# Optimization experiments

Hardware: AMD Instinct MI355X
Metric: run time of the kernel (lower is better)

Reference implementation:

```python
import jax, jax.numpy as jnp
import numpy as np

EMBED = 2048
D_COMPR = 512
D_ROPE = 128
N_HEADS = 8
HEAD_DIM = D_COMPR // N_HEADS  # 64
B, S = 4, 2048


def _lin(x, w, b):
    # torch Linear: y = x @ w.T + b, w: [out, in]
    return jnp.einsum('bsi,oi->bso', x, w) + b


def _rope_emb(seq_len):
    inv_freq = 1.0 / (10000.0 ** (jnp.arange(0, D_ROPE, 2, dtype=jnp.float32) / D_ROPE))
    t = jnp.arange(seq_len, dtype=jnp.float32)
    freqs = jnp.einsum('i,j->ij', t, inv_freq)           # [S, D_ROPE/2]
    return jnp.concatenate([freqs, freqs], axis=-1)      # [S, D_ROPE]


def _apply_rope(x, emb):
    # x: [B, S, D_ROPE], emb: [S, D_ROPE]
    cos, sin = jnp.cos(emb), jnp.sin(emb)
    x1, x2 = jnp.split(x, 2, axis=-1)
    rot = jnp.concatenate([-x2, x1], axis=-1)
    return x * cos + rot * sin


def setup_inputs() -> dict:
    key = jax.random.key(0)
    ks = jax.random.split(key, 20)
    sc = 0.02
    inp = {'x': jax.random.normal(ks[0], (B, S, EMBED), dtype=jnp.float32)}
    def w(k, o, i):
        return jax.random.normal(k, (o, i), dtype=jnp.float32) * sc
    inp['CQ_w'] = w(ks[1], D_COMPR, EMBED); inp['CQ_b'] = jnp.zeros((D_COMPR,), jnp.float32)
    inp['CQC_w'] = w(ks[2], D_COMPR - D_ROPE, D_COMPR); inp['CQC_b'] = jnp.zeros((D_COMPR - D_ROPE,), jnp.float32)
    inp['CQR_w'] = w(ks[3], D_ROPE, EMBED); inp['CQR_b'] = jnp.zeros((D_ROPE,), jnp.float32)
    inp['CKV_w'] = w(ks[4], D_COMPR, EMBED); inp['CKV_b'] = jnp.zeros((D_COMPR,), jnp.float32)
    inp['CKR_w'] = w(ks[5], D_ROPE, EMBED); inp['CKR_b'] = jnp.zeros((D_ROPE,), jnp.float32)
    inp['CKC_w'] = w(ks[6], D_COMPR - D_ROPE, D_COMPR); inp['CKC_b'] = jnp.zeros((D_COMPR - D_ROPE,), jnp.float32)
    inp['CV_w'] = w(ks[7], D_COMPR, D_COMPR); inp['CV_b'] = jnp.zeros((D_COMPR,), jnp.float32)
    inp['OUT_w'] = w(ks[8], EMBED, D_COMPR); inp['OUT_b'] = jnp.zeros((EMBED,), jnp.float32)
    return inp


def reference(x, CQ_w, CQ_b, CQC_w, CQC_b, CQR_w, CQR_b, CKV_w, CKV_b,
              CKR_w, CKR_b, CKC_w, CKC_b, CV_w, CV_b, OUT_w, OUT_b):
    b, s, _ = x.shape
    gelu = lambda t: jax.nn.gelu(t, approximate=False)

    cq = gelu(_lin(x, CQ_w, CQ_b))                # [B,S,D_COMPR]
    cqc = _lin(cq, CQC_w, CQC_b)                  # [B,S,D_COMPR-D_ROPE]
    cqr = _lin(x, CQR_w, CQR_b)                   # [B,S,D_ROPE]
    ckv = gelu(_lin(x, CKV_w, CKV_b))             # [B,S,D_COMPR]
    ckr = _lin(x, CKR_w, CKR_b)                   # [B,S,D_ROPE]
    ckc = _lin(ckv, CKC_w, CKC_b)                 # [B,S,D_COMPR-D_ROPE]

    emb = _rope_emb(s)
    cqr = _apply_rope(cqr, emb)
    ckr = _apply_rope(ckr, emb)

    Q = gelu(jnp.concatenate([cqc, cqr], axis=-1))  # [B,S,D_COMPR]
    K = gelu(jnp.concatenate([ckc, ckr], axis=-1))
    V = _lin(ckv, CV_w, CV_b)

    Q = Q.reshape(b, s, N_HEADS, HEAD_DIM).transpose(0, 2, 1, 3)  # [B,H,S,D]
    K = K.reshape(b, s, N_HEADS, HEAD_DIM).transpose(0, 2, 1, 3)
    V = V.reshape(b, s, N_HEADS, HEAD_DIM).transpose(0, 2, 1, 3)

    scale = 1.0 / np.sqrt(HEAD_DIM).astype(np.float32)
    scores = jnp.einsum('bhqd,bhkd->bhqk', Q, K) * scale
    causal = jnp.triu(jnp.ones((s, s), dtype=bool), k=1)
    scores = jnp.where(causal[None, None], -jnp.inf, scores)
    attn = jax.nn.softmax(scores, axis=-1)
    out = jnp.einsum('bhqk,bhkd->bhqd', attn, V)
    out = out.transpose(0, 2, 1, 3).reshape(b, s, D_COMPR)
    return _lin(out, OUT_w, OUT_b)
```

## Files before the change

kernel.cpp:

```cpp
#include <hip/hip_runtime.h>
#include <cstdint>
#include <cstddef>

typedef unsigned short u16;
typedef short bf16x8 __attribute__((ext_vector_type(8)));
typedef float f32x4 __attribute__((ext_vector_type(4)));
typedef unsigned short u16x8 __attribute__((ext_vector_type(8)));

#define DEVINL __device__ __forceinline__

DEVINL u16 f2bf(float f) {
  union { float f; unsigned u; } v; v.f = f;
  unsigned r = v.u + 0x7FFFu + ((v.u >> 16) & 1u);
  return (u16)(r >> 16);
}
DEVINL float bf2f(u16 h) {
  union { unsigned u; float f; } v; v.u = ((unsigned)h) << 16;
  return v.f;
}
DEVINL float gelu_exact(float x) {
  return 0.5f * x * (1.0f + erff(x * 0.70710678118654752f));
}
DEVINL void gload_lds16(const void* g, void* l) {
  __builtin_amdgcn_global_load_lds(
      (const __attribute__((address_space(1))) void*)g,
      (__attribute__((address_space(3))) void*)l, 16, 0, 0);
}
DEVINL bf16x8 ld_frag(const u16* p) {
  return *reinterpret_cast<const bf16x8*>(p);
}

__global__ __launch_bounds__(256) void conv_f32_bf16(
    const float* __restrict__ src, u16* __restrict__ dst, int n4) {
  int i = blockIdx.x * 256 + threadIdx.x;
  int stride = gridDim.x * 256;
  for (; i < n4; i += stride) {
    float4 v = reinterpret_cast<const float4*>(src)[i];
    ushort4 o;
    o.x = f2bf(v.x); o.y = f2bf(v.y); o.z = f2bf(v.z); o.w = f2bf(v.w);
    reinterpret_cast<ushort4*>(dst)[i] = o;
  }
}

struct EpiSeg {
  const float* bias;
  void* dst;
  int stride;
  int col_start;
  int do_gelu;
};
struct EpiTable { EpiSeg s[4]; int nseg; };

template <int F32OUT>
__global__ __launch_bounds__(256) void gemm_bt(
    const u16* __restrict__ A, const u16* __restrict__ W, int K, EpiTable et) {
  __shared__ u16 As[128 * 32];
  __shared__ u16 Bs[128 * 32];
  const int tid = threadIdx.x;
  const int lane = tid & 63;
  const int wv = tid >> 6;
  const int g = lane >> 4;
  const int c = lane & 15;
  const int wr = (wv >> 1) * 64;
  const int wc = (wv & 1) * 64;
  const long long rowBase = (long long)blockIdx.x * 128;
  const long long colBase = (long long)blockIdx.y * 128;

  f32x4 acc[4][4];
#pragma unroll
  for (int m = 0; m < 4; ++m)
#pragma unroll
    for (int n = 0; n < 4; ++n) acc[m][n] = {0.f, 0.f, 0.f, 0.f};

  const int r0 = tid >> 2, sp0 = tid & 3;
  const int scol = (sp0 ^ ((r0 >> 1) & 3)) * 8;
  const u16* Ag = A + (rowBase + r0) * K + scol;
  const u16* Wg = W + (colBase + r0) * K + scol;
  u16* Al0 = As + tid * 8;
  u16* Al1 = As + (256 + tid) * 8;
  u16* Bl0 = Bs + tid * 8;
  u16* Bl1 = Bs + (256 + tid) * 8;
  const long long skip = 64LL * K;

  int aoff[4], boff[4];
#pragma unroll
  for (int m = 0; m < 4; ++m) {
    int row = wr + m * 16 + c;
    aoff[m] = row * 32 + ((g ^ ((row >> 1) & 3)) * 8);
    int rowb = wc + m * 16 + c;
    boff[m] = rowb * 32 + ((g ^ ((rowb >> 1) & 3)) * 8);
  }

  const int nk = K >> 5;
  for (int kt = 0; kt < nk; ++kt) {
    const int k0 = kt * 32;
    gload_lds16(Ag + k0, Al0);
    gload_lds16(Ag + skip + k0, Al1);
    gload_lds16(Wg + k0, Bl0);
    gload_lds16(Wg + skip + k0, Bl1);
    __syncthreads();
    bf16x8 a[4], b[4];
#pragma unroll
    for (int m = 0; m < 4; ++m) a[m] = ld_frag(&As[aoff[m]]);
#pragma unroll
    for (int n = 0; n < 4; ++n) b[n] = ld_frag(&Bs[boff[n]]);
#pragma unroll
    for (int m = 0; m < 4; ++m)
#pragma unroll
      for (int n = 0; n < 4; ++n)
        acc[m][n] = __builtin_amdgcn_mfma_f32_16x16x32_bf16(a[m], b[n], acc[m][n], 0, 0, 0);
    __syncthreads();
  }

  EpiSeg e = et.s[0];
#pragma unroll
  for (int i = 1; i < 4; ++i)
    if (i < et.nseg && (int)colBase >= et.s[i].col_start) e = et.s[i];

#pragma unroll
  for (int m = 0; m < 4; ++m) {
#pragma unroll
    for (int n = 0; n < 4; ++n) {
      int col = (int)colBase + wc + n * 16 + c;
      int dcol = col - e.col_start;
      float bias = e.bias[dcol];
#pragma unroll
      for (int r = 0; r < 4; ++r) {
        long long row = rowBase + wr + m * 16 + g * 4 + r;
        float v = acc[m][n][r] + bias;
        if (e.do_gelu) v = gelu_exact(v);
        if (F32OUT)
          ((float*)e.dst)[row * e.stride + dcol] = v;
        else
          ((u16*)e.dst)[row * e.stride + dcol] = f2bf(v);
      }
    }
  }
}

__global__ __launch_bounds__(256) void rope_gelu_k(
    const u16* __restrict__ cqr, const u16* __restrict__ ckr,
    u16* __restrict__ Qb, u16* __restrict__ Kb) {
  int idx = blockIdx.x * 256 + threadIdx.x;
  int row = idx >> 6, j = idx & 63;
  int s = row & 2047;
  float invf = exp2f(-(float)j * (13.287712379549449f / 64.f));
  float th = (float)s * invf;
  float sn, cs;
  sincosf(th, &sn, &cs);
  long long r128 = (long long)row * 128;
  float q1 = bf2f(cqr[r128 + j]), q2 = bf2f(cqr[r128 + 64 + j]);
  float k1 = bf2f(ckr[r128 + j]), k2 = bf2f(ckr[r128 + 64 + j]);
  float qo1 = q1 * cs - q2 * sn, qo2 = q2 * cs + q1 * sn;
  float ko1 = k1 * cs - k2 * sn, ko2 = k2 * cs + k1 * sn;
  long long rb = (long long)row * 512;
  Qb[rb + 384 + j] = f2bf(gelu_exact(qo1));
  Qb[rb + 448 + j] = f2bf(gelu_exact(qo2));
  Kb[rb + 384 + j] = f2bf(gelu_exact(ko1));
  Kb[rb + 448 + j] = f2bf(gelu_exact(ko2));
}

__global__ __launch_bounds__(256) void attn_fwd(
    const u16* __restrict__ Q, const u16* __restrict__ Kin,
    const u16* __restrict__ V, u16* __restrict__ O) {
  const int qt = blockIdx.x;
  const int bh = blockIdx.y;
  const int b = bh >> 3, h = bh & 7;
  const int tid = threadIdx.x, lane = tid & 63, wv = tid >> 6;
  const int g = lane >> 4, c = lane & 15;

  __shared__ u16 Ks[64 * 64];
  __shared__ u16 Vt[64 * 72];
  __shared__ u16 Ps[128 * 72];

  const long long rowB = (long long)b * 2048;
  const int qbase = qt * 128;
  const u16* Qp = Q + (rowB + qbase) * 512 + h * 64;
  const u16* Kp = Kin + rowB * 512 + h * 64;
  const u16* Vp = V + rowB * 512 + h * 64;

  bf16x8 qa[2][2];
#pragma unroll
  for (int m = 0; m < 2; ++m)
#pragma unroll
    for (int kc = 0; kc < 2; ++kc)
      qa[m][kc] = ld_frag(Qp + (long long)(wv * 32 + m * 16 + c) * 512 + kc * 32 + g * 8);

  f32x4 o[2][4];
  float mrow[2][4], lrow[2][4];
#pragma unroll
  for (int m = 0; m < 2; ++m) {
#pragma unroll
    for (int nf = 0; nf < 4; ++nf) o[m][nf] = {0.f, 0.f, 0.f, 0.f};
#pragma unroll
    for (int r = 0; r < 4; ++r) { mrow[m][r] = -1e30f; lrow[m][r] = 0.f; }
  }

  const int kr0 = tid >> 3, ksp = tid & 7;
  const int ksrcd = (ksp ^ (kr0 & 7)) * 8;
  const int vkv0 = tid >> 3, vd0 = (tid & 7) * 8;

  const int ntiles = 2 * qt + 2;
  for (int t = 0; t < ntiles; ++t) {
    const int kvb = t * 64;
    gload_lds16(Kp + (long long)(kvb + kr0) * 512 + ksrcd, Ks + tid * 8);
    gload_lds16(Kp + (long long)(kvb + kr0 + 32) * 512 + ksrcd, Ks + (256 + tid) * 8);
    u16x8 v0 = *reinterpret_cast<const u16x8*>(Vp + (long long)(kvb + vkv0) * 512 + vd0);
    u16x8 v1 = *reinterpret_cast<const u16x8*>(Vp + (long long)(kvb + vkv0 + 32) * 512 + vd0);
    __syncthreads();
#pragma unroll
    for (int i = 0; i < 8; ++i) {
      Vt[(vd0 + i) * 72 + vkv0] = v0[i];
      Vt[(vd0 + i) * 72 + vkv0 + 32] = v1[i];
    }
    __syncthreads();

    f32x4 s[2][4];
#pragma unroll
    for (int m = 0; m < 2; ++m)
#pragma unroll
      for (int nf = 0; nf < 4; ++nf) s[m][nf] = {0.f, 0.f, 0.f, 0.f};
#pragma unroll
    for (int kc = 0; kc < 2; ++kc) {
      bf16x8 kb[4];
#pragma unroll
      for (int nf = 0; nf < 4; ++nf) {
        int kvr = nf * 16 + c;
        int slot = (kc * 4 + g) ^ (kvr & 7);
        kb[nf] = ld_frag(&Ks[kvr * 64 + slot * 8]);
      }
#pragma unroll
      for (int m = 0; m < 2; ++m)
#pragma unroll
        for (int nf = 0; nf < 4; ++nf)
          s[m][nf] = __builtin_amdgcn_mfma_f32_16x16x32_bf16(qa[m][kc], kb[nf], s[m][nf], 0, 0, 0);
    }

#pragma unroll
    for (int m = 0; m < 2; ++m) {
#pragma unroll
      for (int r = 0; r < 4; ++r) {
        int qrow = qbase + wv * 32 + m * 16 + g * 4 + r;
        float vmax = -1e30f;
#pragma unroll
        for (int nf = 0; nf < 4; ++nf) {
          int kvcol = kvb + nf * 16 + c;
          float sv = s[m][nf][r] * 0.125f;
          if (kvcol > qrow) sv = -1e30f;
          s[m][nf][r] = sv;
          vmax = fmaxf(vmax, sv);
        }
#pragma unroll
        for (int sh = 1; sh < 16; sh <<= 1)
          vmax = fmaxf(vmax, __shfl_xor(vmax, sh, 64));
        float mo = mrow[m][r];
        float mn = fmaxf(mo, vmax);
        float corr = __expf(mo - mn);
        float psum = 0.f;
#pragma unroll
        for (int nf = 0; nf < 4; ++nf) {
          float p = __expf(s[m][nf][r] - mn);
          s[m][nf][r] = p;
          psum += p;
        }
#pragma unroll
        for (int sh = 1; sh < 16; sh <<= 1)
          psum += __shfl_xor(psum, sh, 64);
        mrow[m][r] = mn;
        lrow[m][r] = lrow[m][r] * corr + psum;
#pragma unroll
        for (int nf = 0; nf < 4; ++nf) o[m][nf][r] *= corr;
      }
    }

#pragma unroll
    for (int m = 0; m < 2; ++m)
#pragma unroll
      for (int nf = 0; nf < 4; ++nf)
#pragma unroll
        for (int r = 0; r < 4; ++r)
          Ps[(wv * 32 + m * 16 + g * 4 + r) * 72 + nf * 16 + c] = f2bf(s[m][nf][r]);
    __syncthreads();

#pragma unroll
    for (int kc2 = 0; kc2 < 2; ++kc2) {
      bf16x8 pa[2], vb[4];
#pragma unroll
      for (int m = 0; m < 2; ++m)
        pa[m] = ld_frag(&Ps[(wv * 32 + m * 16 + c) * 72 + kc2 * 32 + g * 8]);
#pragma unroll
      for (int nf = 0; nf < 4; ++nf)
        vb[nf] = ld_frag(&Vt[(nf * 16 + c) * 72 + kc2 * 32 + g * 8]);
#pragma unroll
      for (int m = 0; m < 2; ++m)
#pragma unroll
        for (int nf = 0; nf < 4; ++nf)
          o[m][nf] = __builtin_amdgcn_mfma_f32_16x16x32_bf16(pa[m], vb[nf], o[m][nf], 0, 0, 0);
    }
  }

#pragma unroll
  for (int m = 0; m < 2; ++m)
#pragma unroll
    for (int r = 0; r < 4; ++r) {
      float inv = 1.0f / lrow[m][r];
      long long row = rowB + qbase + wv * 32 + m * 16 + g * 4 + r;
#pragma unroll
      for (int nf = 0; nf < 4; ++nf) {
        int col = h * 64 + nf * 16 + c;
        O[row * 512 + col] = f2bf(o[m][nf][r] * inv);
      }
    }
}

extern "C" void kernel_launch(void* const* d_in, const int* in_sizes, int n_in,
                              void* d_out, int out_size, void* d_ws, size_t ws_size,
                              hipStream_t stream) {
  const float* x = (const float*)d_in[0];
  const float* CQ_w = (const float*)d_in[1];   const float* CQ_b = (const float*)d_in[2];
  const float* CQC_w = (const float*)d_in[3];  const float* CQC_b = (const float*)d_in[4];
  const float* CQR_w = (const float*)d_in[5];  const float* CQR_b = (const float*)d_in[6];
  const float* CKV_w = (const float*)d_in[7];  const float* CKV_b = (const float*)d_in[8];
  const float* CKR_w = (const float*)d_in[9];  const float* CKR_b = (const float*)d_in[10];
  const float* CKC_w = (const float*)d_in[11]; const float* CKC_b = (const float*)d_in[12];
  const float* CV_w = (const float*)d_in[13];  const float* CV_b = (const float*)d_in[14];
  const float* OUT_w = (const float*)d_in[15]; const float* OUT_b = (const float*)d_in[16];
  float* out = (float*)d_out;

  char* ws = (char*)d_ws;
  size_t off = 0;
  auto alloc = [&](size_t bytes) -> void* {
    void* p = ws + off;
    off += (bytes + 255) & ~(size_t)255;
    return p;
  };
  u16* xb   = (u16*)alloc(8192ULL * 2048 * 2);
  u16* Wc1  = (u16*)alloc(1280ULL * 2048 * 2);
  u16* Wcqc = (u16*)alloc(384ULL * 512 * 2);
  u16* Wc2  = (u16*)alloc(896ULL * 512 * 2);
  u16* Wout = (u16*)alloc(2048ULL * 512 * 2);
  u16* cq   = (u16*)alloc(8192ULL * 512 * 2);
  u16* ckv  = (u16*)alloc(8192ULL * 512 * 2);
  u16* cqrt = (u16*)alloc(8192ULL * 128 * 2);
  u16* ckrt = (u16*)alloc(8192ULL * 128 * 2);
  u16* Qb   = (u16*)alloc(8192ULL * 512 * 2);
  u16* Kbf  = (u16*)alloc(8192ULL * 512 * 2);
  u16* Vb   = (u16*)alloc(8192ULL * 512 * 2);
  u16* AO   = (u16*)alloc(8192ULL * 512 * 2);
  (void)ws_size; (void)in_sizes; (void)n_in; (void)out_size;

  auto conv = [&](const float* s, u16* d, long long n) {
    long long n4 = n / 4;
    int blocks = (int)((n4 + 255) / 256);
    if (blocks > 2048) blocks = 2048;
    conv_f32_bf16<<<blocks, 256, 0, stream>>>(s, d, (int)n4);
  };
  conv(x, xb, 8192LL * 2048);
  conv(CQ_w,  Wc1,                 512LL * 2048);
  conv(CKV_w, Wc1 + 512 * 2048,    512LL * 2048);
  conv(CQR_w, Wc1 + 1024 * 2048,   128LL * 2048);
  conv(CKR_w, Wc1 + 1152 * 2048,   128LL * 2048);
  conv(CQC_w, Wcqc, 384LL * 512);
  conv(CKC_w, Wc2, 384LL * 512);
  conv(CV_w,  Wc2 + 384 * 512, 512LL * 512);
  conv(OUT_w, Wout, 2048LL * 512);

  EpiTable t1 = {};
  t1.nseg = 4;
  t1.s[0] = { CQ_b,  cq,   512, 0,    1 };
  t1.s[1] = { CKV_b, ckv,  512, 512,  1 };
  t1.s[2] = { CQR_b, cqrt, 128, 1024, 0 };
  t1.s[3] = { CKR_b, ckrt, 128, 1152, 0 };
  gemm_bt<0><<<dim3(64, 10), 256, 0, stream>>>(xb, Wc1, 2048, t1);

  rope_gelu_k<<<dim3(8192 * 64 / 256), 256, 0, stream>>>(cqrt, ckrt, Qb, Kbf);

  EpiTable t2 = {};
  t2.nseg = 1;
  t2.s[0] = { CQC_b, Qb, 512, 0, 1 };
  gemm_bt<0><<<dim3(64, 3), 256, 0, stream>>>(cq, Wcqc, 512, t2);

  EpiTable t3 = {};
  t3.nseg = 2;
  t3.s[0] = { CKC_b, Kbf, 512, 0, 1 };
  t3.s[1] = { CV_b,  Vb,  512, 384, 0 };
  gemm_bt<0><<<dim3(64, 7), 256, 0, stream>>>(ckv, Wc2, 512, t3);

  attn_fwd<<<dim3(16, 32), 256, 0, stream>>>(Qb, Kbf, Vb, AO);

  EpiTable t4 = {};
  t4.nseg = 1;
  t4.s[0] = { OUT_b, out, 2048, 0, 0 };
  gemm_bt<1><<<dim3(64, 16), 256, 0, stream>>>(AO, Wout, 512, t4);
}
```

Measured before the change: 468.9 us.

## Balance causal attention by pairing query tiles, fuse weight conversions, swizzle GEMM blocks

The attention kernel now gives each block two 64-row query tiles, p and 31-p, so every block processes the same number of KV tiles. This evens out the causal triangle workload, and the causal mask is applied only on diagonal tiles. Softmax switches to exp2 with the log2e factor folded into the scale. The eight weight conversion launches are merged into one table-driven kernel, and GEMM workgroup ids are remapped to improve L2 locality. The cost is more per-tile branching and a smaller query tile per wave.

Result: faster. 447.7 us (-4.5%).

```diff
diff --git a/kernel.cpp b/kernel.cpp
--- a/kernel.cpp
+++ b/kernel.cpp
@@ -35,6 +35,30 @@
   int i = blockIdx.x * 256 + threadIdx.x;
   int stride = gridDim.x * 256;
   for (; i < n4; i += stride) {
+    float4 v = reinterpret_cast<const float4*>(src)[i];
+    ushort4 o;
+    o.x = f2bf(v.x); o.y = f2bf(v.y); o.z = f2bf(v.z); o.w = f2bf(v.w);
+    reinterpret_cast<ushort4*>(dst)[i] = o;
+  }
+}
+
+struct ConvTab {
+  const float* src[8];
+  u16* dst[8];
+  int bstart[8];
+};
+__global__ __launch_bounds__(256) void conv_w_fused(ConvTab t) {
+  int blk = blockIdx.x;
+  int seg = 0;
+#pragma unroll
+  for (int i = 1; i < 8; ++i)
+    if (blk >= t.bstart[i]) seg = i;
+  const float* src = t.src[seg];
+  u16* dst = t.dst[seg];
+  int base = (blk - t.bstart[seg]) * 1024 + threadIdx.x;
+#pragma unroll
+  for (int k = 0; k < 4; ++k) {
+    int i = base + k * 256;
     float4 v = reinterpret_cast<const float4*>(src)[i];
     ushort4 o;
     o.x = f2bf(v.x); o.y = f2bf(v.y); o.z = f2bf(v.z); o.w = f2bf(v.w);
@@ -63,8 +87,20 @@
   const int c = lane & 15;
   const int wr = (wv >> 1) * 64;
   const int wc = (wv & 1) * 64;
-  const long long rowBase = (long long)blockIdx.x * 128;
-  const long long colBase = (long long)blockIdx.y * 128;
+
+  int bx = blockIdx.x, by = blockIdx.y;
+  {
+    int nwg = gridDim.x * gridDim.y;
+    if ((nwg & 7) == 0) {
+      int lid = by * gridDim.x + bx;
+      int qq = nwg >> 3;
+      int swz = (lid & 7) * qq + (lid >> 3);
+      bx = swz % gridDim.x;
+      by = swz / gridDim.x;
+    }
+  }
+  const long long rowBase = (long long)bx * 128;
+  const long long colBase = (long long)by * 128;
 
   f32x4 acc[4][4];
 #pragma unroll
@@ -163,7 +199,7 @@
 __global__ __launch_bounds__(256) void attn_fwd(
     const u16* __restrict__ Q, const u16* __restrict__ Kin,
     const u16* __restrict__ V, u16* __restrict__ O) {
-  const int qt = blockIdx.x;
+  const int p = blockIdx.x;
   const int bh = blockIdx.y;
   const int b = bh >> 3, h = bh & 7;
   const int tid = threadIdx.x, lane = tid & 63, wv = tid >> 6;
@@ -171,40 +207,43 @@
 
   __shared__ u16 Ks[64 * 64];
   __shared__ u16 Vt[64 * 72];
-  __shared__ u16 Ps[128 * 72];
+  __shared__ u16 Ps[2][64 * 72];
 
   const long long rowB = (long long)b * 2048;
-  const int qbase = qt * 128;
-  const u16* Qp = Q + (rowB + qbase) * 512 + h * 64;
+  const int qb[2] = { p * 64, (31 - p) * 64 };
   const u16* Kp = Kin + rowB * 512 + h * 64;
   const u16* Vp = V + rowB * 512 + h * 64;
 
   bf16x8 qa[2][2];
 #pragma unroll
-  for (int m = 0; m < 2; ++m)
+  for (int tl = 0; tl < 2; ++tl) {
+    const u16* Qp = Q + (rowB + qb[tl] + wv * 16 + c) * 512 + h * 64;
 #pragma unroll
     for (int kc = 0; kc < 2; ++kc)
-      qa[m][kc] = ld_frag(Qp + (long long)(wv * 32 + m * 16 + c) * 512 + kc * 32 + g * 8);
+      qa[tl][kc] = ld_frag(Qp + kc * 32 + g * 8);
+  }
 
   f32x4 o[2][4];
-  float mrow[2][4], lrow[2][4];
-#pragma unroll
-  for (int m = 0; m < 2; ++m) {
-#pragma unroll
-    for (int nf = 0; nf < 4; ++nf) o[m][nf] = {0.f, 0.f, 0.f, 0.f};
-#pragma unroll
-    for (int r = 0; r < 4; ++r) { mrow[m][r] = -1e30f; lrow[m][r] = 0.f; }
+  float m_[2][4], l_[2][4];
+#pragma unroll
+  for (int tl = 0; tl < 2; ++tl) {
+#pragma unroll
+    for (int nf = 0; nf < 4; ++nf) o[tl][nf] = {0.f, 0.f, 0.f, 0.f};
+#pragma unroll
+    for (int r = 0; r < 4; ++r) { m_[tl][r] = -1e30f; l_[tl][r] = 0.f; }
   }
 
   const int kr0 = tid >> 3, ksp = tid & 7;
-  const int ksrcd = (ksp ^ (kr0 & 7)) * 8;
+  const int ksrc = (ksp ^ (kr0 & 7)) * 8;
   const int vkv0 = tid >> 3, vd0 = (tid & 7) * 8;
-
-  const int ntiles = 2 * qt + 2;
-  for (int t = 0; t < ntiles; ++t) {
+  const float SCL2 = 0.18033688011112042f;
+
+  const int nt = 32 - p;
+  for (int t = 0; t < nt; ++t) {
     const int kvb = t * 64;
-    gload_lds16(Kp + (long long)(kvb + kr0) * 512 + ksrcd, Ks + tid * 8);
-    gload_lds16(Kp + (long long)(kvb + kr0 + 32) * 512 + ksrcd, Ks + (256 + tid) * 8);
+    const bool doA = (t <= p);
+    gload_lds16(Kp + (long long)(kvb + kr0) * 512 + ksrc, Ks + tid * 8);
+    gload_lds16(Kp + (long long)(kvb + kr0 + 32) * 512 + ksrc, Ks + (256 + tid) * 8);
     u16x8 v0 = *reinterpret_cast<const u16x8*>(Vp + (long long)(kvb + vkv0) * 512 + vd0);
     u16x8 v1 = *reinterpret_cast<const u16x8*>(Vp + (long long)(kvb + vkv0 + 32) * 512 + vd0);
     __syncthreads();
@@ -217,9 +256,9 @@
 
     f32x4 s[2][4];
 #pragma unroll
-    for (int m = 0; m < 2; ++m)
-#pragma unroll
-      for (int nf = 0; nf < 4; ++nf) s[m][nf] = {0.f, 0.f, 0.f, 0.f};
+    for (int tl = 0; tl < 2; ++tl)
+#pragma unroll
+      for (int nf = 0; nf < 4; ++nf) s[tl][nf] = {0.f, 0.f, 0.f, 0.f};
 #pragma unroll
     for (int kc = 0; kc < 2; ++kc) {
       bf16x8 kb[4];
@@ -230,87 +269,89 @@
         kb[nf] = ld_frag(&Ks[kvr * 64 + slot * 8]);
       }
 #pragma unroll
-      for (int m = 0; m < 2; ++m)
+      for (int nf = 0; nf < 4; ++nf)
+        s[1][nf] = __builtin_amdgcn_mfma_f32_16x16x32_bf16(qa[1][kc], kb[nf], s[1][nf], 0, 0, 0);
+      if (doA) {
 #pragma unroll
         for (int nf = 0; nf < 4; ++nf)
-          s[m][nf] = __builtin_amdgcn_mfma_f32_16x16x32_bf16(qa[m][kc], kb[nf], s[m][nf], 0, 0, 0);
-    }
-
-#pragma unroll
-    for (int m = 0; m < 2; ++m) {
+          s[0][nf] = __builtin_amdgcn_mfma_f32_16x16x32_bf16(qa[0][kc], kb[nf], s[0][nf], 0, 0, 0);
+      }
+    }
+
+#pragma unroll
+    for (int tl = 0; tl < 2; ++tl) {
+      if (tl == 0 && !doA) continue;
+      const bool diag = (tl == 0) ? (t == p) : (t == nt - 1);
+      const int qr0 = qb[tl] + wv * 16 + g * 4;
 #pragma unroll
       for (int r = 0; r < 4; ++r) {
-        int qrow = qbase + wv * 32 + m * 16 + g * 4 + r;
         float vmax = -1e30f;
 #pragma unroll
         for (int nf = 0; nf < 4; ++nf) {
-          int kvcol = kvb + nf * 16 + c;
-          float sv = s[m][nf][r] * 0.125f;
-          if (kvcol > qrow) sv = -1e30f;
-          s[m][nf][r] = sv;
+          float sv = s[tl][nf][r] * SCL2;
+          if (diag && (kvb + nf * 16 + c > qr0 + r)) sv = -1e30f;
+          s[tl][nf][r] = sv;
           vmax = fmaxf(vmax, sv);
         }
 #pragma unroll
         for (int sh = 1; sh < 16; sh <<= 1)
           vmax = fmaxf(vmax, __shfl_xor(vmax, sh, 64));
-        float mo = mrow[m][r];
+        float mo = m_[tl][r];
         float mn = fmaxf(mo, vmax);
-        float corr = __expf(mo - mn);
-        float psum = 0.f;
+        float corr = exp2f(mo - mn);
+        float ps = 0.f;
 #pragma unroll
         for (int nf = 0; nf < 4; ++nf) {
-          float p = __expf(s[m][nf][r] - mn);
-          s[m][nf][r] = p;
-          psum += p;
+          float pv = exp2f(s[tl][nf][r] - mn);
+          s[tl][nf][r] = pv;
+          ps += pv;
         }
 #pragma unroll
         for (int sh = 1; sh < 16; sh <<= 1)
-          psum += __shfl_xor(psum, sh, 64);
-        mrow[m][r] = mn;
-        lrow[m][r] = lrow[m][r] * corr + psum;
-#pragma unroll
-        for (int nf = 0; nf < 4; ++nf) o[m][nf][r] *= corr;
+          ps += __shfl_xor(ps, sh, 64);
+        m_[tl][r] = mn;
+        l_[tl][r] = l_[tl][r] * corr + ps;
+#pragma unroll
+        for (int nf = 0; nf < 4; ++nf) o[tl][nf][r] *= corr;
       }
-    }
-
-#pragma unroll
-    for (int m = 0; m < 2; ++m)
 #pragma unroll
       for (int nf = 0; nf < 4; ++nf)
 #pragma unroll
         for (int r = 0; r < 4; ++r)
-          Ps[(wv * 32 + m * 16 + g * 4 + r) * 72 + nf * 16 + c] = f2bf(s[m][nf][r]);
+          Ps[tl][(wv * 16 + g * 4 + r) * 72 + nf * 16 + c] = f2bf(s[tl][nf][r]);
+    }
     __syncthreads();
 
 #pragma unroll
     for (int kc2 = 0; kc2 < 2; ++kc2) {
-      bf16x8 pa[2], vb[4];
-#pragma unroll
-      for (int m = 0; m < 2; ++m)
-        pa[m] = ld_frag(&Ps[(wv * 32 + m * 16 + c) * 72 + kc2 * 32 + g * 8]);
+      bf16x8 vb[4];
 #pragma unroll
       for (int nf = 0; nf < 4; ++nf)
         vb[nf] = ld_frag(&Vt[(nf * 16 + c) * 72 + kc2 * 32 + g * 8]);
-#pragma unroll
-      for (int m = 0; m < 2; ++m)
+      bf16x8 pb = ld_frag(&Ps[1][(wv * 16 + c) * 72 + kc2 * 32 + g * 8]);
+#pragma unroll
+      for (int nf = 0; nf < 4; ++nf)
+        o[1][nf] = __builtin_amdgcn_mfma_f32_16x16x32_bf16(pb, vb[nf], o[1][nf], 0, 0, 0);
+      if (doA) {
+        bf16x8 pa = ld_frag(&Ps[0][(wv * 16 + c) * 72 + kc2 * 32 + g * 8]);
 #pragma unroll
         for (int nf = 0; nf < 4; ++nf)
-          o[m][nf] = __builtin_amdgcn_mfma_f32_16x16x32_bf16(pa[m], vb[nf], o[m][nf], 0, 0, 0);
-    }
-  }
-
-#pragma unroll
-  for (int m = 0; m < 2; ++m)
+          o[0][nf] = __builtin_amdgcn_mfma_f32_16x16x32_bf16(pa, vb[nf], o[0][nf], 0, 0, 0);
+      }
+    }
+  }
+
+#pragma unroll
+  for (int tl = 0; tl < 2; ++tl) {
 #pragma unroll
     for (int r = 0; r < 4; ++r) {
-      float inv = 1.0f / lrow[m][r];
-      long long row = rowB + qbase + wv * 32 + m * 16 + g * 4 + r;
-#pragma unroll
-      for (int nf = 0; nf < 4; ++nf) {
-        int col = h * 64 + nf * 16 + c;
-        O[row * 512 + col] = f2bf(o[m][nf][r] * inv);
-      }
-    }
+      float inv = 1.0f / l_[tl][r];
+      long long row = rowB + qb[tl] + wv * 16 + g * 4 + r;
+#pragma unroll
+      for (int nf = 0; nf < 4; ++nf)
+        O[row * 512 + h * 64 + nf * 16 + c] = f2bf(o[tl][nf][r] * inv);
+    }
+  }
 }
 
 extern "C" void kernel_launch(void* const* d_in, const int* in_sizes, int n_in,
@@ -330,9 +371,9 @@
   char* ws = (char*)d_ws;
   size_t off = 0;
   auto alloc = [&](size_t bytes) -> void* {
-    void* p = ws + off;
+    void* pp = ws + off;
     off += (bytes + 255) & ~(size_t)255;
-    return p;
+    return pp;
   };
   u16* xb   = (u16*)alloc(8192ULL * 2048 * 2);
   u16* Wc1  = (u16*)alloc(1280ULL * 2048 * 2);
@@ -349,21 +390,21 @@
   u16* AO   = (u16*)alloc(8192ULL * 512 * 2);
   (void)ws_size; (void)in_sizes; (void)n_in; (void)out_size;
 
-  auto conv = [&](const float* s, u16* d, long long n) {
-    long long n4 = n / 4;
-    int blocks = (int)((n4 + 255) / 256);
-    if (blocks > 2048) blocks = 2048;
-    conv_f32_bf16<<<blocks, 256, 0, stream>>>(s, d, (int)n4);
-  };
-  conv(x, xb, 8192LL * 2048);
-  conv(CQ_w,  Wc1,                 512LL * 2048);
-  conv(CKV_w, Wc1 + 512 * 2048,    512LL * 2048);
-  conv(CQR_w, Wc1 + 1024 * 2048,   128LL * 2048);
-  conv(CKR_w, Wc1 + 1152 * 2048,   128LL * 2048);
-  conv(CQC_w, Wcqc, 384LL * 512);
-  conv(CKC_w, Wc2, 384LL * 512);
-  conv(CV_w,  Wc2 + 384 * 512, 512LL * 512);
-  conv(OUT_w, Wout, 2048LL * 512);
+  conv_f32_bf16<<<2048, 256, 0, stream>>>(x, xb, 8192 * 2048 / 4);
+
+  ConvTab ct;
+  ct.src[0] = CQ_w;  ct.dst[0] = Wc1;
+  ct.src[1] = CKV_w; ct.dst[1] = Wc1 + 512 * 2048;
+  ct.src[2] = CQR_w; ct.dst[2] = Wc1 + 1024 * 2048;
+  ct.src[3] = CKR_w; ct.dst[3] = Wc1 + 1152 * 2048;
+  ct.src[4] = CQC_w; ct.dst[4] = Wcqc;
+  ct.src[5] = CKC_w; ct.dst[5] = Wc2;
+  ct.src[6] = CV_w;  ct.dst[6] = Wc2 + 384 * 512;
+  ct.src[7] = OUT_w; ct.dst[7] = Wout;
+  int bs = 0;
+  int nblk[8] = {256, 256, 64, 64, 48, 48, 64, 256};
+  for (int i = 0; i < 8; ++i) { ct.bstart[i] = bs; bs += nblk[i]; }
+  conv_w_fused<<<bs, 256, 0, stream>>>(ct);
 
   EpiTable t1 = {};
   t1.nseg = 4;
```
